# Kernel tuning notes

Hardware: AMD Instinct MI355X
Metric: run time of the kernel (lower is better)

The kernel has to match this reference:

```python
import jax, jax.numpy as jnp
import numpy as np

VMF_KAPPA = 30.0      # vMF concentration
THRESHOLD = 0.0       # vc_thresholds
OCC_LIKELY = 0.6      # occ_likely[0]
NUM_MIXTURES = 4
EPS_L1 = 1e-12        # torch F.normalize eps


def _l1_normalize(x, axis):
    n = jnp.sum(jnp.abs(x), axis=axis, keepdims=True)
    return x / jnp.maximum(n, EPS_L1)


def _crop_or_pad(mm, H, W):
    # center crop or zero-pad mix model spatial dims to (H, W); shapes are static
    _, _, hm, wm = mm.shape
    if hm < H:
        d1 = (H - hm) // 2
        mm = jnp.pad(mm, ((0, 0), (0, 0), (d1, H - hm - d1), (0, 0)))
    elif hm > H:
        d1 = (hm - H) // 2
        mm = mm[:, :, d1:d1 + H, :]
    if wm < W:
        d1 = (W - wm) // 2
        mm = jnp.pad(mm, ((0, 0), (0, 0), (0, 0), (d1, W - wm - d1)))
    elif wm > W:
        d1 = (wm - W) // 2
        mm = mm[:, :, :, d1:d1 + W]
    return mm


def setup_inputs() -> dict:
    key = jax.random.key(0)
    k1, k2, k3, k4 = jax.random.split(key, 4)
    B, C, H, W = 32, 512, 56, 56
    VC = 512              # number of vMF codebook vectors
    KM = 48               # num_classes(12) * num_mixtures(4)
    NCLUT = 5             # clutter models
    return {
        "vgg_feat": jax.random.normal(k1, (B, C, H, W), dtype=jnp.float32),
        "conv_weight": jax.random.normal(k2, (VC, C, 1, 1), dtype=jnp.float32),
        "mix_model": jax.random.uniform(k3, (KM, VC, H, W), dtype=jnp.float32),
        "clutter_model": jax.random.uniform(k4, (NCLUT, VC), dtype=jnp.float32),
    }


def reference(vgg_feat, conv_weight, mix_model, clutter_model):
    B, C, H, W = vgg_feat.shape
    # --- Conv1o1: cosine similarity between L2-normalized features and codebook ---
    xnorm = jnp.linalg.norm(vgg_feat, axis=1, keepdims=True)
    xnorm = xnorm + (xnorm == 0).astype(vgg_feat.dtype)  # avoid div-by-zero
    xn = vgg_feat / xnorm
    w = conv_weight[:, :, 0, 0]                           # (vc, C) 1x1 kernel
    wn = w / jnp.linalg.norm(w, axis=1, keepdims=True)
    cos = jnp.einsum('bchw,kc->bkhw', xn, wn)             # (B, vc, H, W)
    # --- vMF activation ---
    act = jnp.exp(VMF_KAPPA * cos) * (cos > THRESHOLD).astype(cos.dtype)
    # --- PointwiseInferenceLayer (vmf, use_mixture_bg=True) ---
    ck = _l1_normalize(jnp.clip(clutter_model, 0.0, 1.0), axis=1)  # (N, vc)
    bg = jnp.einsum('bkhw,nk->bnhw', act, ck)                      # (B, N, H, W)
    background = jnp.log(bg * OCC_LIKELY + 1e-10)
    background = jnp.max(background, axis=1, keepdims=True)        # (B, 1, H, W)
    background = background[:, None, None]                         # (B,1,1,1,H,W)

    mm = _l1_normalize(jnp.clip(mix_model, 0.0, 1.0), axis=1)      # (KM, vc, Hm, Wm)
    mm = _crop_or_pad(mm, H, W)
    fg = jnp.einsum('bkhw,mkhw->bmhw', act, mm)                    # (B, KM, H, W)
    foreground = jnp.log(fg * (1.0 - OCC_LIKELY) + 1e-10)
    num_classes = mm.shape[0] // NUM_MIXTURES
    foreground = foreground.reshape(B, num_classes, NUM_MIXTURES, 1, H, W)
    per_model = jnp.maximum(foreground, background).sum(axis=(-1, -2))  # (B,K,M,1)
    scores = per_model.max(axis=-1).max(axis=-1)                        # (B, K)
    mix_likeli = scores / (H * W)
    # SoftMaxTemp(2.0)
    z = jnp.exp(jnp.clip(mix_likeli * 2.0, -88.7, 88.7))
    soft = z / jnp.sum(z, axis=1, keepdims=True)
    return soft, vgg_feat, mix_likeli
```

## Files before the change

### kernel.cpp

```cpp
#include <hip/hip_runtime.h>

#define B_ 32
#define C_ 512
#define HW_ 3136
#define KF_ 512
#define KM_ 48
#define NCL_ 5

typedef __attribute__((ext_vector_type(8))) short short8;
typedef __attribute__((ext_vector_type(4))) short short4v;
typedef __attribute__((ext_vector_type(4))) float floatx4;
typedef unsigned int u32;
typedef u32 __attribute__((address_space(1))) gu32;
typedef u32 __attribute__((address_space(3))) lu32;

__device__ __forceinline__ unsigned short f2bf(float f) {
    union { float f; unsigned u; } v; v.f = f;
    unsigned r = v.u + 0x7FFFu + ((v.u >> 16) & 1u);
    return (unsigned short)(r >> 16);
}
__device__ __forceinline__ float bf2f(unsigned short u) {
    union { unsigned u; float f; } v; v.u = ((unsigned)u) << 16;
    return v.f;
}
__device__ __forceinline__ void gl2lds16(const void* g, void* l) {
    __builtin_amdgcn_global_load_lds((const gu32*)g, (lu32*)l, 16, 0, 0);
}
__device__ __forceinline__ void gl2lds4(const void* g, void* l) {
    __builtin_amdgcn_global_load_lds((const gu32*)g, (lu32*)l, 4, 0, 0);
}

__global__ __launch_bounds__(64) void prep_kernel(const float* __restrict__ w,
                                                  const float* __restrict__ cl,
                                                  unsigned short* __restrict__ wn,
                                                  float* __restrict__ ck) {
    int bid = blockIdx.x, t = threadIdx.x;
    if (bid < KF_) {
        const float* row = w + (size_t)bid * C_;
        float ss = 0.f;
        float x[8];
#pragma unroll
        for (int j = 0; j < 8; ++j) { x[j] = row[t * 8 + j]; ss += x[j] * x[j]; }
        for (int m = 32; m >= 1; m >>= 1) ss += __shfl_xor(ss, m);
        float inv = 1.f / sqrtf(ss);
#pragma unroll
        for (int j = 0; j < 8; ++j) wn[(size_t)bid * C_ + t * 8 + j] = f2bf(x[j] * inv);
    } else {
        int n = bid - KF_;
        if (n >= NCL_) return;
        const float* row = cl + (size_t)n * KF_;
        float s = 0.f;
        float v[8];
#pragma unroll
        for (int j = 0; j < 8; ++j) {
            float x = row[t * 8 + j];
            x = fminf(fmaxf(x, 0.f), 1.f);
            v[j] = x; s += x;
        }
        for (int m = 32; m >= 1; m >>= 1) s += __shfl_xor(s, m);
        float inv = 1.f / fmaxf(s, 1e-12f);
#pragma unroll
        for (int j = 0; j < 8; ++j) ck[(size_t)n * KF_ + t * 8 + j] = v[j] * inv;
    }
}

__global__ __launch_bounds__(512) void xprep_kernel(const float* __restrict__ vgg,
                                                    unsigned short* __restrict__ xnt,
                                                    float* __restrict__ invn,
                                                    float* __restrict__ out_vgg,
                                                    int write_vgg) {
    int pt = blockIdx.x, b = blockIdx.y;
    int tid = threadIdx.x;
    int px = tid & 63, cq = tid >> 6;
    __shared__ __align__(16) unsigned short tile[64][512];
    __shared__ float ssp[8][64];
    const float* vcol = vgg + (size_t)b * C_ * HW_ + pt * 64 + px;
    float* ovcol = out_vgg + (size_t)b * C_ * HW_ + pt * 64 + px;

    float ss = 0.f;
#pragma unroll
    for (int j = 0; j < 16; ++j) {
        int c0 = cq * 64 + j * 4;
        float x0 = vcol[(size_t)(c0 + 0) * HW_];
        float x1 = vcol[(size_t)(c0 + 1) * HW_];
        float x2 = vcol[(size_t)(c0 + 2) * HW_];
        float x3 = vcol[(size_t)(c0 + 3) * HW_];
        ss += x0 * x0 + x1 * x1 + x2 * x2 + x3 * x3;
        short4v pk;
        pk[0] = (short)f2bf(x0); pk[1] = (short)f2bf(x1);
        pk[2] = (short)f2bf(x2); pk[3] = (short)f2bf(x3);
        *(short4v*)&tile[px][c0] = pk;
        if (write_vgg) {
            ovcol[(size_t)(c0 + 0) * HW_] = x0;
            ovcol[(size_t)(c0 + 1) * HW_] = x1;
            ovcol[(size_t)(c0 + 2) * HW_] = x2;
            ovcol[(size_t)(c0 + 3) * HW_] = x3;
        }
    }
    ssp[cq][px] = ss;
    __syncthreads();
    if (tid < 64) {
        float s = 0.f;
#pragma unroll
        for (int q = 0; q < 8; ++q) s += ssp[q][tid];
        float n = sqrtf(s);
        invn[(size_t)b * HW_ + pt * 64 + tid] = (n == 0.f) ? 1.f : 1.f / n;
    }
    __syncthreads();
    int row = tid >> 3, ch = tid & 7;
    unsigned short* orow = xnt + ((size_t)b * HW_ + pt * 64 + row) * 512;
#pragma unroll
    for (int j = 0; j < 8; ++j) {
        int c8 = (ch + 8 * j) * 8;
        *(short8*)(orow + c8) = *(const short8*)&tile[row][c8];
    }
}

__global__ __launch_bounds__(256) void gemm_act_kernel(const unsigned short* __restrict__ xnt,
                                                       const unsigned short* __restrict__ wn,
                                                       const float* __restrict__ invn,
                                                       const float* __restrict__ ck,
                                                       unsigned short* __restrict__ act,
                                                       float* __restrict__ bgacc) {
    int ft = blockIdx.x, pt = blockIdx.y;
    int tid = threadIdx.x, lane = tid & 63, w = tid >> 6;
    int wm = w & 1, wq = w >> 1;
    __shared__ __align__(16) unsigned short a_lds[128 * 64];
    __shared__ __align__(16) unsigned short b_lds[128 * 64];
    __shared__ float ck_l[NCL_ * KF_];
    __shared__ float inv_l[128];
    __shared__ float bga_l[128 * NCL_];

    for (int i = tid; i < NCL_ * KF_; i += 256) ck_l[i] = ck[i];
    if (tid < 128) inv_l[tid] = invn[(size_t)pt * 128 + tid];
    for (int i = tid; i < 128 * NCL_; i += 256) bga_l[i] = 0.f;

    const unsigned short* ga = wn + ((size_t)(ft * 128) + (tid >> 3)) * 512 + (tid & 7) * 8;
    const unsigned short* gb = xnt + ((size_t)pt * 128 + (tid >> 3)) * 512 + (tid & 7) * 8;
    unsigned short* la = a_lds + (tid >> 3) * 64 + (tid & 7) * 8;
    unsigned short* lb = b_lds + (tid >> 3) * 64 + (tid & 7) * 8;

    floatx4 acc[4][4] = {};
    for (int ks = 0; ks < 8; ++ks) {
#pragma unroll
        for (int s = 0; s < 4; ++s) {
            gl2lds16(ga + (size_t)s * 32 * 512 + ks * 64, la + s * 32 * 64);
            gl2lds16(gb + (size_t)s * 32 * 512 + ks * 64, lb + s * 32 * 64);
        }
        __syncthreads();
#pragma unroll
        for (int k2 = 0; k2 < 2; ++k2) {
            short8 af[4], bf[4];
#pragma unroll
            for (int i = 0; i < 4; ++i) {
                af[i] = *(const short8*)&a_lds[(wm * 64 + i * 16 + (lane & 15)) * 64 + k2 * 32 + (lane >> 4) * 8];
                bf[i] = *(const short8*)&b_lds[(wq * 64 + i * 16 + (lane & 15)) * 64 + k2 * 32 + (lane >> 4) * 8];
            }
#pragma unroll
            for (int mi = 0; mi < 4; ++mi)
#pragma unroll
                for (int ni = 0; ni < 4; ++ni)
                    acc[mi][ni] = __builtin_amdgcn_mfma_f32_16x16x32_bf16(af[mi], bf[ni], acc[mi][ni], 0, 0, 0);
        }
        __syncthreads();
    }

#pragma unroll
    for (int ni = 0; ni < 4; ++ni) {
        int px_l = wq * 64 + ni * 16 + (lane & 15);
        float inv = inv_l[px_l];
        size_t row_g = (size_t)pt * 128 + px_l;
        float bp[NCL_] = {0.f, 0.f, 0.f, 0.f, 0.f};
#pragma unroll
        for (int mi = 0; mi < 4; ++mi) {
            int f_g = ft * 128 + wm * 64 + mi * 16 + (lane >> 4) * 4;
            int chn = ft * 8 + wm * 4 + mi;
            int kin = (lane >> 4) * 4;
            short4v pk;
            float av[4];
#pragma unroll
            for (int r = 0; r < 4; ++r) {
                float cv = acc[mi][ni][r] * inv;
                float a = cv > 0.f ? __expf(30.f * cv) : 0.f;
                av[r] = a;
                pk[r] = (short)f2bf(a);
            }
            *(short4v*)(act + ((size_t)chn * 100352 + row_g) * 16 + kin) = pk;
#pragma unroll
            for (int n = 0; n < NCL_; ++n)
                bp[n] += av[0] * ck_l[n * KF_ + f_g] + av[1] * ck_l[n * KF_ + f_g + 1] +
                         av[2] * ck_l[n * KF_ + f_g + 2] + av[3] * ck_l[n * KF_ + f_g + 3];
        }
#pragma unroll
        for (int n = 0; n < NCL_; ++n) {
            float v = bp[n];
            v += __shfl_xor(v, 16);
            v += __shfl_xor(v, 32);
            if ((lane >> 4) == 0) atomicAdd(&bga_l[px_l * NCL_ + n], v);
        }
    }
    __syncthreads();
    if (tid < 128) {
        size_t row_g = (size_t)pt * 128 + tid;
#pragma unroll
        for (int n = 0; n < NCL_; ++n)
            atomicAdd(&bgacc[row_g * 8 + n], bga_l[tid * NCL_ + n]);
    }
}

#define MMBUF 50112
#define ACTBUF 16640
#define OFF_ACT0 (2*MMBUF)
#define OFF_CSUM (2*MMBUF + 2*ACTBUF)
#define OFF_PMS  (OFF_CSUM + 3072)
#define OFF_BGS  (OFF_PMS + 6144)
__global__ __launch_bounds__(1024) void fg_kernel(const unsigned short* __restrict__ act,
                                                  const float* __restrict__ mm,
                                                  const float* __restrict__ bgacc,
                                                  float* __restrict__ pm) {
    __shared__ __align__(16) unsigned char L[OFF_BGS + 2048];
    float* csum_s = (float*)(L + OFF_CSUM);
    float* pms    = (float*)(L + OFF_PMS);
    float* bgs    = (float*)(L + OFF_BGS);

    int p0 = blockIdx.x * 16;
    int tid = threadIdx.x;
    int lane = tid & 63, wid = tid >> 6;
    int li = lane & 15, q = lane >> 4;
    int pp = wid;
    int w3 = wid * 3;

    for (int i = tid; i < 1536; i += 1024) pms[i] = 0.f;
    if (tid < 512) {
        int b = tid >> 4, px = tid & 15;
        const float* bga = bgacc + ((size_t)b * HW_ + p0 + px) * 8;
        float mx = -1e30f;
#pragma unroll
        for (int n = 0; n < NCL_; ++n) mx = fmaxf(mx, logf(bga[n] * 0.6f + 1e-10f));
        bgs[tid] = mx;
    }

    const float* mm_src = mm + ((size_t)(w3 * KF_) + (size_t)(lane >> 4)) * HW_ + p0 + (lane & 15);
    const unsigned short* act_src = act +
        ((size_t)(2 * wid + (lane >> 5)) * HW_ + p0 + ((lane >> 1) & 15)) * 16 + (lane & 1) * 8;

    auto stage = [&](int s) {
        unsigned char* mb = L + (s & 1) * MMBUF;
        unsigned char* ab = L + OFF_ACT0 + (s & 1) * ACTBUF;
        const float* ms = mm_src + (size_t)s * 16 * HW_;
#pragma unroll
        for (int jj = 0; jj < 12; ++jj)
            gl2lds4(ms + (size_t)((jj >> 2) * KF_ + (jj & 3) * 4) * HW_,
                    mb + (w3 + (jj >> 2)) * 1044 + (jj & 3) * 256);
        gl2lds16(act_src + (size_t)s * 100352 * 16, ab + wid * 1040);
    };

    short8 fa[2] = {};
    short8 fmA[3] = {};
    floatx4 acc[3][2] = {};
    float csp[3] = {0.f, 0.f, 0.f};

    stage(0);
    __syncthreads();

#pragma unroll 2
    for (int s = 0; s < 32; ++s) {
        if (s < 31) stage(s + 1);
        const unsigned char* mc = L + (s & 1) * MMBUF;
        const unsigned char* ac = L + OFF_ACT0 + (s & 1) * ACTBUF;
        if ((q >> 1) == (s & 1)) {
#pragma unroll
            for (int bf = 0; bf < 2; ++bf)
                fa[bf] = *(const short8*)(ac + (bf * 8 + (li >> 1)) * 1040 +
                                          ((li & 1) * 16 + pp) * 32 + (q & 1) * 16);
#pragma unroll
            for (int mf = 0; mf < 3; ++mf) {
                const unsigned char* arow = mc + (mf * 16 + li) * 1044 + (q & 1) * 512 + pp * 4;
                short8 pk;
                float s0 = 0.f;
#pragma unroll
                for (int j = 0; j < 8; ++j) {
                    float x = *(const float*)(arow + j * 64);
                    x = fminf(fmaxf(x, 0.f), 1.f);
                    s0 += x;
                    pk[j] = (short)f2bf(x);
                }
                csp[mf] += s0;
                fmA[mf] = pk;
            }
        }
        if (s & 1) {
#pragma unroll
            for (int mf = 0; mf < 3; ++mf) {
                acc[mf][0] = __builtin_amdgcn_mfma_f32_16x16x32_bf16(fmA[mf], fa[0], acc[mf][0], 0, 0, 0);
                acc[mf][1] = __builtin_amdgcn_mfma_f32_16x16x32_bf16(fmA[mf], fa[1], acc[mf][1], 0, 0, 0);
            }
        }
        __syncthreads();
    }

#pragma unroll
    for (int mf = 0; mf < 3; ++mf) {
        float v = csp[mf];
        v += __shfl_xor(v, 16);
        v += __shfl_xor(v, 32);
        if (q == 0) csum_s[(mf * 16 + li) * 16 + pp] = v;
    }
    __syncthreads();

#pragma unroll
    for (int mf = 0; mf < 3; ++mf)
#pragma unroll
        for (int bf = 0; bf < 2; ++bf) {
            int b = bf * 16 + li;
            float bgv = bgs[b * 16 + pp];
#pragma unroll
            for (int r = 0; r < 4; ++r) {
                int m = mf * 16 + q * 4 + r;
                float inv = 1.f / fmaxf(csum_s[m * 16 + pp], 1e-12f);
                float v = fmaxf(logf(acc[mf][bf][r] * inv * 0.4f + 1e-10f), bgv);
                atomicAdd(&pms[m * 32 + b], v);
            }
        }
    __syncthreads();
    if (tid < 512) {
        int i3 = tid * 3;
#pragma unroll
        for (int j = 0; j < 3; ++j) {
            int i = i3 + j;
            int m = i >> 5, b = i & 31;
            atomicAdd(&pm[(size_t)b * KM_ + m], pms[i]);
        }
    }
}

__global__ __launch_bounds__(64) void final_kernel(const float* __restrict__ pm,
                                                   float* __restrict__ out_soft,
                                                   float* __restrict__ out_ml) {
    int b = threadIdx.x;
    if (b >= B_) return;
    float ml[12];
#pragma unroll
    for (int c = 0; c < 12; ++c) {
        float s = -1e30f;
#pragma unroll
        for (int j = 0; j < 4; ++j) s = fmaxf(s, pm[(size_t)b * KM_ + c * 4 + j]);
        ml[c] = s / (float)HW_;
    }
    float z[12], zs = 0.f;
#pragma unroll
    for (int c = 0; c < 12; ++c) {
        float e = fminf(fmaxf(ml[c] * 2.f, -88.7f), 88.7f);
        z[c] = expf(e); zs += z[c];
    }
#pragma unroll
    for (int c = 0; c < 12; ++c) {
        out_soft[(size_t)b * 12 + c] = z[c] / zs;
        out_ml[(size_t)b * 12 + c] = ml[c];
    }
}

extern "C" void kernel_launch(void* const* d_in, const int* in_sizes, int n_in,
                              void* d_out, int out_size, void* d_ws, size_t ws_size,
                              hipStream_t stream) {
    const float* vgg = (const float*)d_in[0];
    const float* cw  = (const float*)d_in[1];
    const float* mmp = (const float*)d_in[2];
    const float* cl  = (const float*)d_in[3];
    float* out = (float*)d_out;
    char* ws = (char*)d_ws;

    unsigned short* wn   = (unsigned short*)(ws);
    float* ck            = (float*)(ws + 524288);
    float* invn          = (float*)(ws + 534528);
    float* pm            = (float*)(ws + 935936);
    float* bgacc         = (float*)(ws + 942080);
    unsigned short* xnt  = (unsigned short*)(ws + 4153344);
    const size_t ACT_OFF = 4153344 + 102760448;
    const size_t ACT_BYTES = (size_t)B_ * HW_ * KF_ * 2;

    int big_ws = (ws_size >= ACT_OFF + ACT_BYTES) ? 1 : 0;
    unsigned short* act = big_ws ? (unsigned short*)(ws + ACT_OFF)
                                 : (unsigned short*)(out + 384);

    hipMemsetAsync(pm, 0, (size_t)B_ * KM_ * sizeof(float), stream);
    hipMemsetAsync(bgacc, 0, (size_t)B_ * HW_ * 8 * sizeof(float), stream);
    prep_kernel<<<dim3(KF_ + NCL_), dim3(64), 0, stream>>>(cw, cl, wn, ck);
    xprep_kernel<<<dim3(49, 32), dim3(512), 0, stream>>>(vgg, xnt, invn, out + 384, big_ws);
    gemm_act_kernel<<<dim3(4, 784), dim3(256), 0, stream>>>(xnt, wn, invn, ck, act, bgacc);
    fg_kernel<<<dim3(196), dim3(1024), 0, stream>>>(act, mmp, bgacc, pm);
    final_kernel<<<1, 64, 0, stream>>>(pm, out, out + 384 + (size_t)B_ * C_ * HW_);
    if (!big_ws)
        hipMemcpyAsync(out + 384, vgg, (size_t)B_ * C_ * HW_ * sizeof(float),
                       hipMemcpyDeviceToDevice, stream);
}
```

Measured before the change: 469.7 us.

## Move clutter background reduction into fg kernel MFMA and double-buffer GEMM

The clutter/background dot product leaves the GEMM epilogue, which used scalar FMAs, LDS atomics and global atomics into a bgacc buffer. It is now computed as extra bf16 MFMAs inside fg_kernel, using a padded bf16 clutter matrix staged in LDS. This also removes the bgacc memset. gemm_act_kernel moves to 512 threads with double-buffered LDS prefetch and a swizzled 1D grid. The cost is bf16 precision for the clutter weights and larger LDS use in both kernels.

Measured after the change: 405.9 us. -13.6%, faster.

```diff
diff --git a/kernel.cpp b/kernel.cpp
--- a/kernel.cpp
+++ b/kernel.cpp
@@ -33,7 +33,7 @@
 __global__ __launch_bounds__(64) void prep_kernel(const float* __restrict__ w,
                                                   const float* __restrict__ cl,
                                                   unsigned short* __restrict__ wn,
-                                                  float* __restrict__ ck) {
+                                                  unsigned short* __restrict__ ckb) {
     int bid = blockIdx.x, t = threadIdx.x;
     if (bid < KF_) {
         const float* row = w + (size_t)bid * C_;
@@ -47,20 +47,25 @@
         for (int j = 0; j < 8; ++j) wn[(size_t)bid * C_ + t * 8 + j] = f2bf(x[j] * inv);
     } else {
         int n = bid - KF_;
-        if (n >= NCL_) return;
-        const float* row = cl + (size_t)n * KF_;
-        float s = 0.f;
-        float v[8];
-#pragma unroll
-        for (int j = 0; j < 8; ++j) {
-            float x = row[t * 8 + j];
-            x = fminf(fmaxf(x, 0.f), 1.f);
-            v[j] = x; s += x;
-        }
-        for (int m = 32; m >= 1; m >>= 1) s += __shfl_xor(s, m);
-        float inv = 1.f / fmaxf(s, 1e-12f);
-#pragma unroll
-        for (int j = 0; j < 8; ++j) ck[(size_t)n * KF_ + t * 8 + j] = v[j] * inv;
+        if (n >= 16) return;
+        if (n < NCL_) {
+            const float* row = cl + (size_t)n * KF_;
+            float s = 0.f;
+            float v[8];
+#pragma unroll
+            for (int j = 0; j < 8; ++j) {
+                float x = row[t * 8 + j];
+                x = fminf(fmaxf(x, 0.f), 1.f);
+                v[j] = x; s += x;
+            }
+            for (int m = 32; m >= 1; m >>= 1) s += __shfl_xor(s, m);
+            float inv = 1.f / fmaxf(s, 1e-12f);
+#pragma unroll
+            for (int j = 0; j < 8; ++j) ckb[(size_t)n * KF_ + t * 8 + j] = f2bf(v[j] * inv);
+        } else {
+#pragma unroll
+            for (int j = 0; j < 8; ++j) ckb[(size_t)n * KF_ + t * 8 + j] = 0;
+        }
     }
 }
 
@@ -116,95 +121,82 @@
     }
 }
 
-__global__ __launch_bounds__(256) void gemm_act_kernel(const unsigned short* __restrict__ xnt,
+__global__ __launch_bounds__(512) void gemm_act_kernel(const unsigned short* __restrict__ xnt,
                                                        const unsigned short* __restrict__ wn,
                                                        const float* __restrict__ invn,
-                                                       const float* __restrict__ ck,
-                                                       unsigned short* __restrict__ act,
-                                                       float* __restrict__ bgacc) {
-    int ft = blockIdx.x, pt = blockIdx.y;
-    int tid = threadIdx.x, lane = tid & 63, w = tid >> 6;
-    int wm = w & 1, wq = w >> 1;
-    __shared__ __align__(16) unsigned short a_lds[128 * 64];
-    __shared__ __align__(16) unsigned short b_lds[128 * 64];
-    __shared__ float ck_l[NCL_ * KF_];
+                                                       unsigned short* __restrict__ act) {
+    int wg = blockIdx.x;
+    int swz = (wg & 7) * 392 + (wg >> 3);
+    int pt = swz >> 2, ft = swz & 3;
+    int tid = threadIdx.x, lane = tid & 63;
+    int wid = tid >> 6;
+    int li = lane & 15, q = lane >> 4;
+    int wm = wid & 1, wq = wid >> 1;
+
+    __shared__ __align__(16) unsigned short a_lds[2][128 * 64];
+    __shared__ __align__(16) unsigned short b_lds[2][128 * 64];
     __shared__ float inv_l[128];
-    __shared__ float bga_l[128 * NCL_];
-
-    for (int i = tid; i < NCL_ * KF_; i += 256) ck_l[i] = ck[i];
     if (tid < 128) inv_l[tid] = invn[(size_t)pt * 128 + tid];
-    for (int i = tid; i < 128 * NCL_; i += 256) bga_l[i] = 0.f;
-
-    const unsigned short* ga = wn + ((size_t)(ft * 128) + (tid >> 3)) * 512 + (tid & 7) * 8;
+
+    const unsigned short* ga = wn + ((size_t)ft * 128 + (tid >> 3)) * 512 + (tid & 7) * 8;
     const unsigned short* gb = xnt + ((size_t)pt * 128 + (tid >> 3)) * 512 + (tid & 7) * 8;
-    unsigned short* la = a_lds + (tid >> 3) * 64 + (tid & 7) * 8;
-    unsigned short* lb = b_lds + (tid >> 3) * 64 + (tid & 7) * 8;
-
-    floatx4 acc[4][4] = {};
-    for (int ks = 0; ks < 8; ++ks) {
-#pragma unroll
-        for (int s = 0; s < 4; ++s) {
-            gl2lds16(ga + (size_t)s * 32 * 512 + ks * 64, la + s * 32 * 64);
-            gl2lds16(gb + (size_t)s * 32 * 512 + ks * 64, lb + s * 32 * 64);
+    int ldst = tid * 8;
+
+    floatx4 acc[4][2] = {};
+
+#pragma unroll
+    for (int i = 0; i < 2; ++i) {
+        gl2lds16(ga + (size_t)i * 64 * 512, &a_lds[0][ldst + i * 4096]);
+        gl2lds16(gb + (size_t)i * 64 * 512, &b_lds[0][ldst + i * 4096]);
+    }
+    __syncthreads();
+
+#pragma unroll 1
+    for (int s = 0; s < 8; ++s) {
+        if (s < 7) {
+            int nb = (s + 1) & 1;
+#pragma unroll
+            for (int i = 0; i < 2; ++i) {
+                gl2lds16(ga + (size_t)i * 64 * 512 + (s + 1) * 64, &a_lds[nb][ldst + i * 4096]);
+                gl2lds16(gb + (size_t)i * 64 * 512 + (s + 1) * 64, &b_lds[nb][ldst + i * 4096]);
+            }
+        }
+        int buf = s & 1;
+#pragma unroll
+        for (int k2 = 0; k2 < 2; ++k2) {
+            short8 af[4], bfr[2];
+#pragma unroll
+            for (int i = 0; i < 4; ++i)
+                af[i] = *(const short8*)&a_lds[buf][(wm * 64 + i * 16 + li) * 64 + k2 * 32 + q * 8];
+#pragma unroll
+            for (int j = 0; j < 2; ++j)
+                bfr[j] = *(const short8*)&b_lds[buf][(wq * 32 + j * 16 + li) * 64 + k2 * 32 + q * 8];
+#pragma unroll
+            for (int i = 0; i < 4; ++i)
+#pragma unroll
+                for (int j = 0; j < 2; ++j)
+                    acc[i][j] = __builtin_amdgcn_mfma_f32_16x16x32_bf16(af[i], bfr[j], acc[i][j], 0, 0, 0);
         }
         __syncthreads();
-#pragma unroll
-        for (int k2 = 0; k2 < 2; ++k2) {
-            short8 af[4], bf[4];
-#pragma unroll
-            for (int i = 0; i < 4; ++i) {
-                af[i] = *(const short8*)&a_lds[(wm * 64 + i * 16 + (lane & 15)) * 64 + k2 * 32 + (lane >> 4) * 8];
-                bf[i] = *(const short8*)&b_lds[(wq * 64 + i * 16 + (lane & 15)) * 64 + k2 * 32 + (lane >> 4) * 8];
-            }
-#pragma unroll
-            for (int mi = 0; mi < 4; ++mi)
-#pragma unroll
-                for (int ni = 0; ni < 4; ++ni)
-                    acc[mi][ni] = __builtin_amdgcn_mfma_f32_16x16x32_bf16(af[mi], bf[ni], acc[mi][ni], 0, 0, 0);
-        }
-        __syncthreads();
-    }
-
-#pragma unroll
-    for (int ni = 0; ni < 4; ++ni) {
-        int px_l = wq * 64 + ni * 16 + (lane & 15);
-        float inv = inv_l[px_l];
-        size_t row_g = (size_t)pt * 128 + px_l;
-        float bp[NCL_] = {0.f, 0.f, 0.f, 0.f, 0.f};
-#pragma unroll
-        for (int mi = 0; mi < 4; ++mi) {
-            int f_g = ft * 128 + wm * 64 + mi * 16 + (lane >> 4) * 4;
-            int chn = ft * 8 + wm * 4 + mi;
-            int kin = (lane >> 4) * 4;
+    }
+
+#pragma unroll
+    for (int j = 0; j < 2; ++j) {
+        int px = wq * 32 + j * 16 + li;
+        float inv = inv_l[px];
+        size_t row_g = (size_t)pt * 128 + px;
+#pragma unroll
+        for (int i = 0; i < 4; ++i) {
+            int chn = ft * 8 + wm * 4 + i;
             short4v pk;
-            float av[4];
 #pragma unroll
             for (int r = 0; r < 4; ++r) {
-                float cv = acc[mi][ni][r] * inv;
+                float cv = acc[i][j][r] * inv;
                 float a = cv > 0.f ? __expf(30.f * cv) : 0.f;
-                av[r] = a;
                 pk[r] = (short)f2bf(a);
             }
-            *(short4v*)(act + ((size_t)chn * 100352 + row_g) * 16 + kin) = pk;
-#pragma unroll
-            for (int n = 0; n < NCL_; ++n)
-                bp[n] += av[0] * ck_l[n * KF_ + f_g] + av[1] * ck_l[n * KF_ + f_g + 1] +
-                         av[2] * ck_l[n * KF_ + f_g + 2] + av[3] * ck_l[n * KF_ + f_g + 3];
-        }
-#pragma unroll
-        for (int n = 0; n < NCL_; ++n) {
-            float v = bp[n];
-            v += __shfl_xor(v, 16);
-            v += __shfl_xor(v, 32);
-            if ((lane >> 4) == 0) atomicAdd(&bga_l[px_l * NCL_ + n], v);
-        }
-    }
-    __syncthreads();
-    if (tid < 128) {
-        size_t row_g = (size_t)pt * 128 + tid;
-#pragma unroll
-        for (int n = 0; n < NCL_; ++n)
-            atomicAdd(&bgacc[row_g * 8 + n], bga_l[tid * NCL_ + n]);
+            *(short4v*)(act + ((size_t)chn * 100352 + row_g) * 16 + q * 4) = pk;
+        }
     }
 }
 
@@ -213,15 +205,15 @@
 #define OFF_ACT0 (2*MMBUF)
 #define OFF_CSUM (2*MMBUF + 2*ACTBUF)
 #define OFF_PMS  (OFF_CSUM + 3072)
-#define OFF_BGS  (OFF_PMS + 6144)
+#define OFF_CKB  (OFF_PMS + 6144)
 __global__ __launch_bounds__(1024) void fg_kernel(const unsigned short* __restrict__ act,
                                                   const float* __restrict__ mm,
-                                                  const float* __restrict__ bgacc,
+                                                  const unsigned short* __restrict__ ckb,
                                                   float* __restrict__ pm) {
-    __shared__ __align__(16) unsigned char L[OFF_BGS + 2048];
+    __shared__ __align__(16) unsigned char L[OFF_CKB + 16 * 520 * 2];
     float* csum_s = (float*)(L + OFF_CSUM);
     float* pms    = (float*)(L + OFF_PMS);
-    float* bgs    = (float*)(L + OFF_BGS);
+    unsigned short* ckbl = (unsigned short*)(L + OFF_CKB);
 
     int p0 = blockIdx.x * 16;
     int tid = threadIdx.x;
@@ -231,13 +223,9 @@
     int w3 = wid * 3;
 
     for (int i = tid; i < 1536; i += 1024) pms[i] = 0.f;
-    if (tid < 512) {
-        int b = tid >> 4, px = tid & 15;
-        const float* bga = bgacc + ((size_t)b * HW_ + p0 + px) * 8;
-        float mx = -1e30f;
-#pragma unroll
-        for (int n = 0; n < NCL_; ++n) mx = fmaxf(mx, logf(bga[n] * 0.6f + 1e-10f));
-        bgs[tid] = mx;
+    {
+        int row = tid >> 6, cg = tid & 63;
+        *(short8*)&ckbl[row * 520 + cg * 8] = *(const short8*)(ckb + row * 512 + cg * 8);
     }
 
     const float* mm_src = mm + ((size_t)(w3 * KF_) + (size_t)(lane >> 4)) * HW_ + p0 + (lane & 15);
@@ -257,7 +245,9 @@
 
     short8 fa[2] = {};
     short8 fmA[3] = {};
+    short8 fck = {};
     floatx4 acc[3][2] = {};
+    floatx4 accbg[2] = {};
     float csp[3] = {0.f, 0.f, 0.f};
 
     stage(0);
@@ -288,6 +278,7 @@
                 csp[mf] += s0;
                 fmA[mf] = pk;
             }
+            fck = *(const short8*)&ckbl[li * 520 + s * 16 + (q & 1) * 8];
         }
         if (s & 1) {
 #pragma unroll
@@ -295,6 +286,8 @@
                 acc[mf][0] = __builtin_amdgcn_mfma_f32_16x16x32_bf16(fmA[mf], fa[0], acc[mf][0], 0, 0, 0);
                 acc[mf][1] = __builtin_amdgcn_mfma_f32_16x16x32_bf16(fmA[mf], fa[1], acc[mf][1], 0, 0, 0);
             }
+            accbg[0] = __builtin_amdgcn_mfma_f32_16x16x32_bf16(fck, fa[0], accbg[0], 0, 0, 0);
+            accbg[1] = __builtin_amdgcn_mfma_f32_16x16x32_bf16(fck, fa[1], accbg[1], 0, 0, 0);
         }
         __syncthreads();
     }
@@ -306,6 +299,17 @@
         v += __shfl_xor(v, 32);
         if (q == 0) csum_s[(mf * 16 + li) * 16 + pp] = v;
     }
+
+    float bgv[2];
+#pragma unroll
+    for (int bf = 0; bf < 2; ++bf) {
+        float v = -1e30f;
+#pragma unroll
+        for (int r = 0; r < 4; ++r) v = fmaxf(v, logf(accbg[bf][r] * 0.6f + 1e-10f));
+        v = fmaxf(v, __shfl_xor(v, 16));
+        v = fmaxf(v, __shfl_xor(v, 32));
+        bgv[bf] = v;
+    }
     __syncthreads();
 
 #pragma unroll
@@ -313,12 +317,11 @@
 #pragma unroll
         for (int bf = 0; bf < 2; ++bf) {
             int b = bf * 16 + li;
-            float bgv = bgs[b * 16 + pp];
 #pragma unroll
             for (int r = 0; r < 4; ++r) {
                 int m = mf * 16 + q * 4 + r;
                 float inv = 1.f / fmaxf(csum_s[m * 16 + pp], 1e-12f);
-                float v = fmaxf(logf(acc[mf][bf][r] * inv * 0.4f + 1e-10f), bgv);
+                float v = fmaxf(logf(acc[mf][bf][r] * inv * 0.4f + 1e-10f), bgv[bf]);
                 atomicAdd(&pms[m * 32 + b], v);
             }
         }
@@ -371,12 +374,11 @@
     char* ws = (char*)d_ws;
 
     unsigned short* wn   = (unsigned short*)(ws);
-    float* ck            = (float*)(ws + 524288);
-    float* invn          = (float*)(ws + 534528);
-    float* pm            = (float*)(ws + 935936);
-    float* bgacc         = (float*)(ws + 942080);
-    unsigned short* xnt  = (unsigned short*)(ws + 4153344);
-    const size_t ACT_OFF = 4153344 + 102760448;
+    unsigned short* ckb  = (unsigned short*)(ws + 524288);
+    float* invn          = (float*)(ws + 540672);
+    float* pm            = (float*)(ws + 942080);
+    unsigned short* xnt  = (unsigned short*)(ws + 948224);
+    const size_t ACT_OFF = 948224 + 102760448;
     const size_t ACT_BYTES = (size_t)B_ * HW_ * KF_ * 2;
 
     int big_ws = (ws_size >= ACT_OFF + ACT_BYTES) ? 1 : 0;
@@ -384,11 +386,10 @@
                                  : (unsigned short*)(out + 384);
 
     hipMemsetAsync(pm, 0, (size_t)B_ * KM_ * sizeof(float), stream);
-    hipMemsetAsync(bgacc, 0, (size_t)B_ * HW_ * 8 * sizeof(float), stream);
-    prep_kernel<<<dim3(KF_ + NCL_), dim3(64), 0, stream>>>(cw, cl, wn, ck);
+    prep_kernel<<<dim3(KF_ + 16), dim3(64), 0, stream>>>(cw, cl, wn, ckb);
     xprep_kernel<<<dim3(49, 32), dim3(512), 0, stream>>>(vgg, xnt, invn, out + 384, big_ws);
-    gemm_act_kernel<<<dim3(4, 784), dim3(256), 0, stream>>>(xnt, wn, invn, ck, act, bgacc);
-    fg_kernel<<<dim3(196), dim3(1024), 0, stream>>>(act, mmp, bgacc, pm);
+    gemm_act_kernel<<<dim3(3136), dim3(512), 0, stream>>>(xnt, wn, invn, act);
+    fg_kernel<<<dim3(196), dim3(1024), 0, stream>>>(act, mmp, ckb, pm);
     final_kernel<<<1, 64, 0, stream>>>(pm, out, out + 384 + (size_t)B_ * C_ * HW_);
     if (!big_ws)
         hipMemcpyAsync(out + 384, vgg, (size_t)B_ * C_ * HW_ * sizeof(float),
```
